# Kernel optimization log

Hardware: AMD Instinct MI355X
Metric: run time of the kernel (lower is better)

The kernel has to match this reference:

```python
import jax, jax.numpy as jnp
import numpy as np
from jax import lax

C = 256
HEADS = 8
AREA = 4
MLP_DIM = int(1.2 * C)  # 307


def _conv1x1(x, w, s, b):
    # x: [B,C,H,W], w: [O,C], s,b: [O]  (Conv2d 1x1 bias=False + folded BN)
    y = jnp.einsum('bchw,oc->bohw', x, w)
    return y * s[None, :, None, None] + b[None, :, None, None]


def _dwconv3x3(x, w, s, b):
    # depthwise 3x3, groups=C; w: [C,1,3,3]
    y = lax.conv_general_dilated(x, w, (1, 1), ((1, 1), (1, 1)),
                                 feature_group_count=x.shape[1],
                                 dimension_numbers=('NCHW', 'OIHW', 'NCHW'))
    return y * s[None, :, None, None] + b[None, :, None, None]


def setup_inputs() -> dict:
    key = jax.random.key(0)
    ks = jax.random.split(key, 8)
    B, H, W = 2, 64, 64
    x = jax.random.normal(ks[0], (B, C, H, W), dtype=jnp.float32)
    std = 0.02
    w_qk = jax.random.normal(ks[1], (2 * C, C), dtype=jnp.float32) * std
    w_v = jax.random.normal(ks[2], (C, C), dtype=jnp.float32) * std
    w_pe = jax.random.normal(ks[3], (C, 1, 3, 3), dtype=jnp.float32) * std
    w_proj = jax.random.normal(ks[4], (C, C), dtype=jnp.float32) * std
    w_m1 = jax.random.normal(ks[5], (MLP_DIM, C), dtype=jnp.float32) * std
    w_m2 = jax.random.normal(ks[6], (C, MLP_DIM), dtype=jnp.float32) * std
    ones = lambda n: jnp.ones((n,), jnp.float32)
    zeros = lambda n: jnp.zeros((n,), jnp.float32)
    return {
        'x': x,
        'w_qk': w_qk, 's_qk': ones(2 * C), 'b_qk': zeros(2 * C),
        'w_v': w_v, 's_v': ones(C), 'b_v': zeros(C),
        'w_pe': w_pe, 's_pe': ones(C), 'b_pe': zeros(C),
        'w_proj': w_proj, 's_proj': ones(C), 'b_proj': zeros(C),
        'w_m1': w_m1, 's_m1': ones(MLP_DIM), 'b_m1': zeros(MLP_DIM),
        'w_m2': w_m2, 's_m2': ones(C), 'b_m2': zeros(C),
    }


def _block(x, w_qk, s_qk, b_qk, w_v, s_v, b_v, w_pe, s_pe, b_pe,
           w_proj, s_proj, b_proj, w_m1, s_m1, b_m1, w_m2, s_m2, b_m2):
    B, Cc, H, W = x.shape
    N = H * W
    hd = Cc // HEADS
    scale = hd ** -0.5

    # --- AreaAttention ---
    qk = _conv1x1(x, w_qk, s_qk, b_qk).reshape(B, 2 * Cc, N)
    v4 = _conv1x1(x, w_v, s_v, b_v)                 # [B,C,H,W]
    pe = _dwconv3x3(v4, w_pe, s_pe, b_pe)           # positional encoding
    v = v4.reshape(B, Cc, N)

    # area split (row-major reshape, identical to torch contiguous reshape)
    Ba, Na = B * AREA, N // AREA
    qk = qk.reshape(Ba, 2 * Cc, Na)
    v = v.reshape(Ba, Cc, Na)
    q, k = qk[:, :Cc], qk[:, Cc:]
    q = q.reshape(Ba, HEADS, hd, Na)
    k = k.reshape(Ba, HEADS, hd, Na)
    v = v.reshape(Ba, HEADS, hd, Na)

    attn = jnp.einsum('bhdn,bhdm->bhnm', q, k) * scale  # [Ba,H,Na,Na]
    attn = jax.nn.softmax(attn, axis=-1)
    out = jnp.einsum('bhdm,bhnm->bhdn', v, attn)         # [Ba,H,hd,Na]

    out = out.reshape(B, Cc, N).reshape(B, Cc, H, W)
    attn_out = _conv1x1(out + pe, w_proj, s_proj, b_proj)

    x1 = x + attn_out  # add=True (shortcut and in_c==out_c)

    # --- conv2 MLP: Conv(SiLU) -> Conv(act=False) ---
    m = jax.nn.silu(_conv1x1(x1, w_m1, s_m1, b_m1))
    m = _conv1x1(m, w_m2, s_m2, b_m2)
    return x1 + m


def reference(x, w_qk, s_qk, b_qk, w_v, s_v, b_v, w_pe, s_pe, b_pe,
              w_proj, s_proj, b_proj, w_m1, s_m1, b_m1, w_m2, s_m2, b_m2):
    return _block(x, w_qk, s_qk, b_qk, w_v, s_v, b_v, w_pe, s_pe, b_pe,
                  w_proj, s_proj, b_proj, w_m1, s_m1, b_m1, w_m2, s_m2, b_m2)
```

## Files before the change

### kernel.cpp

```cpp
#include <hip/hip_runtime.h>

typedef __attribute__((ext_vector_type(8))) short s8v;
typedef __attribute__((ext_vector_type(4))) float f4v;

#define QSC (0.17677669529663687f * 1.4426950408889634f)

__device__ __forceinline__ unsigned short f2bf(float x) {
    unsigned u = __float_as_uint(x);
    return (unsigned short)((u + 0x7fffu + ((u >> 16) & 1u)) >> 16);
}
__device__ __forceinline__ float bf2f(unsigned short h) {
    return __uint_as_float(((unsigned)h) << 16);
}
__device__ __forceinline__ unsigned trunc2(float a, float b) {
    return (__float_as_uint(b) & 0xffff0000u) | (__float_as_uint(a) >> 16);
}

__global__ __launch_bounds__(256) void wconv_kernel(
    const float* __restrict__ wqk, const float* __restrict__ sqk, const float* __restrict__ bqk,
    const float* __restrict__ wv,  const float* __restrict__ sv,  const float* __restrict__ bv,
    const float* __restrict__ wprj, const float* __restrict__ sprj,
    const float* __restrict__ wm1, const float* __restrict__ sm1, const float* __restrict__ bm1,
    const float* __restrict__ wm2, const float* __restrict__ sm2,
    unsigned short* __restrict__ Wqkv, unsigned short* __restrict__ Wp,
    unsigned short* __restrict__ Wm1,  unsigned short* __restrict__ Wm2,
    float* __restrict__ bpad, float* __restrict__ bqv)
{
    int i = blockIdx.x * 256 + threadIdx.x;
    if (i < 196608) {
        int o = i >> 8, c = i & 255;
        float w;
        if (o < 512) { float f = ((o & 127) < 64) ? QSC : 1.f; w = wqk[i] * sqk[o] * f; }
        else          w = wv[(o - 512) * 256 + c] * sv[o - 512];
        Wqkv[i] = f2bf(w);
    } else if (i < 262144) {
        int j = i - 196608; int o = j >> 8; Wp[j] = f2bf(wprj[j] * sprj[o]);
    } else if (i < 360448) {
        int j = i - 262144; int o = j >> 8, c = j & 255;
        Wm1[j] = (o < 307) ? f2bf(wm1[o * 256 + c] * sm1[o]) : (unsigned short)0;
    } else if (i < 458752) {
        int j = i - 360448; int o = j / 384, c = j - o * 384;
        Wm2[j] = (c < 307) ? f2bf(wm2[o * 307 + c] * sm2[o]) : (unsigned short)0;
    } else if (i < 459136) {
        int j = i - 458752; bpad[j] = (j < 307) ? bm1[j] : 0.f;
    } else if (i < 459904) {
        int j = i - 459136;
        bqv[j] = (j < 512) ? (bqk[j] * (((j & 127) < 64) ? QSC : 1.f)) : bv[j - 512];
    }
}

__global__ __launch_bounds__(256) void mmqkv_kernel(
    const float* __restrict__ X, const unsigned short* __restrict__ Wb,
    const float* __restrict__ bi,
    unsigned short* __restrict__ qP, unsigned short* __restrict__ kP,
    unsigned short* __restrict__ vC, unsigned short* __restrict__ vT)
{
    __shared__ unsigned short Ap[64][40];
    __shared__ unsigned short Wt[128][40];
    const int tid = threadIdx.x, lane = tid & 63, wv = tid >> 6;
    const int lo4 = lane & 15, quad = lane >> 4;
    const int p0 = blockIdx.x * 64, o0 = blockIdx.y * 128, bB = blockIdx.z;
    const int ph = (wv & 1) * 32, oh = (wv >> 1) * 64;
    const int c2 = tid & 15, pg = tid >> 4;
    const int oW0 = tid >> 2, oW1 = (tid + 256) >> 2;
    const int cW = (tid & 3) * 8;
    const float* xb = X + (size_t)bB * 256 * 4096;

    f4v acc[4][2];
    #pragma unroll
    for (int i = 0; i < 4; i++)
        #pragma unroll
        for (int j = 0; j < 2; j++)
            acc[i][j] = (f4v){0.f, 0.f, 0.f, 0.f};

    float4 fa = *(const float4*)&xb[(size_t)(2 * c2) * 4096 + p0 + pg * 4];
    float4 fb = *(const float4*)&xb[(size_t)(2 * c2 + 1) * 4096 + p0 + pg * 4];
    uint4 wReg0 = *(const uint4*)(Wb + (size_t)(o0 + oW0) * 256 + cW);
    uint4 wReg1 = *(const uint4*)(Wb + (size_t)(o0 + oW1) * 256 + cW);

    for (int kc = 0; kc < 8; kc++) {
        __syncthreads();
        {
            float av[4] = {fa.x, fa.y, fa.z, fa.w};
            float bv2[4] = {fb.x, fb.y, fb.z, fb.w};
            #pragma unroll
            for (int i = 0; i < 4; i++)
                *(unsigned*)&Ap[pg * 4 + i][2 * c2] =
                    (unsigned)f2bf(av[i]) | ((unsigned)f2bf(bv2[i]) << 16);
        }
        *(uint4*)&Wt[oW0][cW] = wReg0;
        *(uint4*)&Wt[oW1][cW] = wReg1;
        __syncthreads();
        if (kc < 7) {
            int k1 = (kc + 1) * 32;
            fa = *(const float4*)&xb[(size_t)(k1 + 2 * c2) * 4096 + p0 + pg * 4];
            fb = *(const float4*)&xb[(size_t)(k1 + 2 * c2 + 1) * 4096 + p0 + pg * 4];
            wReg0 = *(const uint4*)(Wb + (size_t)(o0 + oW0) * 256 + k1 + cW);
            wReg1 = *(const uint4*)(Wb + (size_t)(o0 + oW1) * 256 + k1 + cW);
        }
        s8v af[4], bx[2];
        #pragma unroll
        for (int of = 0; of < 4; of++)
            af[of] = *(const s8v*)&Wt[oh + of * 16 + lo4][quad * 8];
        #pragma unroll
        for (int pf = 0; pf < 2; pf++)
            bx[pf] = *(const s8v*)&Ap[ph + pf * 16 + lo4][quad * 8];
        #pragma unroll
        for (int of = 0; of < 4; of++)
            #pragma unroll
            for (int pf = 0; pf < 2; pf++)
                acc[of][pf] = __builtin_amdgcn_mfma_f32_16x16x32_bf16(af[of], bx[pf], acc[of][pf], 0, 0, 0);
    }
    #pragma unroll
    for (int of = 0; of < 4; of++) {
        int ob = o0 + oh + of * 16 + quad * 4;
        float4 bb = *(const float4*)&bi[ob];
        float bbv[4] = {bb.x, bb.y, bb.z, bb.w};
        #pragma unroll
        for (int pf = 0; pf < 2; pf++) {
            int p = p0 + ph + pf * 16 + lo4;
            unsigned short b4[4];
            #pragma unroll
            for (int r = 0; r < 4; r++) b4[r] = f2bf(acc[of][pf][r] + bbv[r]);
            if (ob < 512) {
                int gg = ob >> 7, rr = ob & 127;
                int hh = (rr & 63) >> 3, j0 = rr & 7;
                unsigned short* dst = (rr >= 64) ? kP : qP;
                *(ushort4*)&dst[((((size_t)(bB * 4 + gg)) * 8 + hh) * 1024 + (p & 1023)) * 32
                                + (p >> 10) * 8 + j0] = *(ushort4*)b4;
            } else {
                *(ushort4*)&vC[((size_t)(bB * 4096 + p)) * 256 + (ob - 512)] = *(ushort4*)b4;
                #pragma unroll
                for (int r = 0; r < 4; r++)
                    vT[((size_t)(bB * 256 + ob - 512 + r)) * 4096 + p] = b4[r];
            }
        }
    }
}

__global__ __launch_bounds__(256) void attn_kernel(
    const unsigned short* __restrict__ qP, const unsigned short* __restrict__ kP,
    const unsigned short* __restrict__ vT,
    unsigned short* __restrict__ Opart, float* __restrict__ Lpart)
{
    __shared__ unsigned short Pq[4][32][72];
    const int tid = threadIdx.x;
    const int w = tid >> 6, lane = tid & 63;
    const int lo4 = lane & 15, quad = lane >> 4;
    const int n0 = blockIdx.z * 128;
    const int h = blockIdx.y;
    const int z = blockIdx.x;
    const int ba = z >> 2, spl = z & 3;
    const int bB = ba >> 2, g = ba & 3;
    const int mbase = spl * 256;

    const unsigned short* qb = qP + (((size_t)(bB * 4) + g) * 8 + h) * 32768;
    const unsigned short* kb = kP + (((size_t)(bB * 4) + g) * 8 + h) * 32768;

    s8v qf[2];
    #pragma unroll
    for (int qc = 0; qc < 2; qc++)
        qf[qc] = *(const s8v*)(qb + (size_t)(n0 + w * 32 + qc * 16 + lo4) * 32 + quad * 8);
    const int dd0 = lo4, dd1 = 16 + lo4;
    const unsigned short* vb0 = vT + ((size_t)(bB * 256 + g * 64 + h * 8 + (dd0 & 7))) * 4096 + (dd0 >> 3) * 1024 + mbase + quad * 8;
    const unsigned short* vb1 = vT + ((size_t)(bB * 256 + g * 64 + h * 8 + (dd1 & 7))) * 4096 + (dd1 >> 3) * 1024 + mbase + quad * 8;

    f4v oacc[2][2], Lacc[2];
    #pragma unroll
    for (int i = 0; i < 2; i++) {
        Lacc[i] = (f4v){0.f, 0.f, 0.f, 0.f};
        #pragma unroll
        for (int j = 0; j < 2; j++)
            oacc[i][j] = (f4v){0.f, 0.f, 0.f, 0.f};
    }
    s8v ones;
    #pragma unroll
    for (int j = 0; j < 8; j++) ones[j] = (short)0x3F80;

    s8v kf[4], vReg[2][2];
    #pragma unroll
    for (int mf = 0; mf < 4; mf++)
        kf[mf] = *(const s8v*)(kb + (size_t)(mbase + mf * 16 + lo4) * 32 + quad * 8);
    #pragma unroll
    for (int mc = 0; mc < 2; mc++) {
        vReg[mc][0] = *(const s8v*)(vb0 + mc * 32);
        vReg[mc][1] = *(const s8v*)(vb1 + mc * 32);
    }

    for (int sc = 0; sc < 4; sc++) {
        s8v kfn[4], vNext[2][2];
        if (sc < 3) {
            #pragma unroll
            for (int mf = 0; mf < 4; mf++)
                kfn[mf] = *(const s8v*)(kb + (size_t)(mbase + (sc + 1) * 64 + mf * 16 + lo4) * 32 + quad * 8);
            #pragma unroll
            for (int mc = 0; mc < 2; mc++) {
                vNext[mc][0] = *(const s8v*)(vb0 + (sc + 1) * 64 + mc * 32);
                vNext[mc][1] = *(const s8v*)(vb1 + (sc + 1) * 64 + mc * 32);
            }
        }
        f4v sT[4][2];
        #pragma unroll
        for (int mf = 0; mf < 4; mf++)
            #pragma unroll
            for (int qc = 0; qc < 2; qc++)
                sT[mf][qc] = __builtin_amdgcn_mfma_f32_16x16x32_bf16(kf[mf], qf[qc], (f4v){0.f, 0.f, 0.f, 0.f}, 0, 0, 0);
        #pragma unroll
        for (int qc = 0; qc < 2; qc++) {
            #pragma unroll
            for (int mf = 0; mf < 4; mf++) {
                float p0v = exp2f(sT[mf][qc][0]);
                float p1v = exp2f(sT[mf][qc][1]);
                float p2v = exp2f(sT[mf][qc][2]);
                float p3v = exp2f(sT[mf][qc][3]);
                uint2 pk;
                pk.x = trunc2(p0v, p1v);
                pk.y = trunc2(p2v, p3v);
                *(uint2*)&Pq[w][qc * 16 + lo4][mf * 16 + quad * 4] = pk;
            }
        }
        #pragma unroll
        for (int mc = 0; mc < 2; mc++) {
            s8v pfr[2];
            #pragma unroll
            for (int qc = 0; qc < 2; qc++)
                pfr[qc] = *(const s8v*)&Pq[w][qc * 16 + lo4][mc * 32 + quad * 8];
            #pragma unroll
            for (int df = 0; df < 2; df++)
                #pragma unroll
                for (int qc = 0; qc < 2; qc++)
                    oacc[df][qc] = __builtin_amdgcn_mfma_f32_16x16x32_bf16(vReg[mc][df], pfr[qc], oacc[df][qc], 0, 0, 0);
            #pragma unroll
            for (int qc = 0; qc < 2; qc++)
                Lacc[qc] = __builtin_amdgcn_mfma_f32_16x16x32_bf16(ones, pfr[qc], Lacc[qc], 0, 0, 0);
        }
        #pragma unroll
        for (int mf = 0; mf < 4; mf++) kf[mf] = kfn[mf];
        #pragma unroll
        for (int mc = 0; mc < 2; mc++) {
            vReg[mc][0] = vNext[mc][0];
            vReg[mc][1] = vNext[mc][1];
        }
    }
    if (quad == 0) {
        size_t lb = (((size_t)(spl * 2 + bB) * 4 + g) * 8 + h) * 1024 + n0 + w * 32;
        Lpart[lb + lo4] = Lacc[0][0];
        Lpart[lb + 16 + lo4] = Lacc[1][0];
    }
    #pragma unroll
    for (int qc = 0; qc < 2; qc++)
        #pragma unroll
        for (int df = 0; df < 2; df++) {
            int pb = df * 2 + (quad >> 1);
            uint2 ov;
            ov.x = trunc2(oacc[df][qc][0], oacc[df][qc][1]);
            ov.y = trunc2(oacc[df][qc][2], oacc[df][qc][3]);
            *(uint2*)(Opart + ((size_t)(spl * 2 + bB) * 4096 + pb * 1024 + n0 + w * 32 + qc * 16 + lo4) * 256
                      + g * 64 + h * 8 + (quad & 1) * 4) = ov;
        }
}

__global__ __launch_bounds__(256) void attpe_kernel(
    const unsigned short* __restrict__ Opart, const float* __restrict__ Lpart,
    const unsigned short* __restrict__ vC, const float* __restrict__ wpe,
    const float* __restrict__ spe, const float* __restrict__ bpe,
    unsigned short* __restrict__ attpe)
{
    int idx = blockIdx.x * 256 + threadIdx.x;
    int cg = (idx & 31) * 8;
    int p = (idx >> 5) & 4095;
    int bB = idx >> 17;
    float L = 0.f;
    float o[8] = {};
    #pragma unroll
    for (int spl = 0; spl < 4; spl++) {
        int g = cg >> 6, h = (cg >> 3) & 7;
        int na = p & 1023;
        L += Lpart[(((size_t)(spl * 2 + bB) * 4 + g) * 8 + h) * 1024 + na];
        uint4 v = *(const uint4*)(Opart + ((size_t)(spl * 2 + bB) * 4096 + p) * 256 + cg);
        unsigned short tmp[8]; *(uint4*)tmp = v;
        #pragma unroll
        for (int j = 0; j < 8; j++) o[j] += bf2f(tmp[j]);
    }
    float inv = 1.f / L;
    int hh = p >> 6, ww = p & 63;
    float pe[8] = {};
    for (int di = -1; di <= 1; di++) {
        int h2 = hh + di;
        if (h2 < 0 || h2 > 63) continue;
        for (int dj = -1; dj <= 1; dj++) {
            int w2 = ww + dj;
            if (w2 < 0 || w2 > 63) continue;
            uint4 vv = *(const uint4*)(vC + ((size_t)(bB * 4096 + h2 * 64 + w2)) * 256 + cg);
            unsigned short tmp[8]; *(uint4*)tmp = vv;
            int k = (di + 1) * 3 + (dj + 1);
            #pragma unroll
            for (int j = 0; j < 8; j++)
                pe[j] = fmaf(bf2f(tmp[j]), wpe[(cg + j) * 9 + k], pe[j]);
        }
    }
    unsigned short ob[8];
    #pragma unroll
    for (int j = 0; j < 8; j++)
        ob[j] = f2bf(o[j] * inv + pe[j] * spe[cg + j] + bpe[cg + j]);
    *(uint4*)(attpe + ((size_t)(bB * 4096 + p)) * 256 + cg) = *(uint4*)ob;
}

__global__ __launch_bounds__(256) void mlp3_kernel(
    const unsigned short* __restrict__ attpe, const float* __restrict__ x,
    const unsigned short* __restrict__ Wp, const float* __restrict__ bp,
    const unsigned short* __restrict__ Wm1, const float* __restrict__ bm1p,
    const unsigned short* __restrict__ Wm2, const float* __restrict__ bm2,
    float* __restrict__ out)
{
    __shared__ unsigned short bufA[32][392];
    __shared__ unsigned short bufX[32][264];
    const int tid = threadIdx.x, lane = tid & 63, wv = tid >> 6;
    const int lo4 = lane & 15, quad = lane >> 4;
    const int p0 = blockIdx.x * 32, bB = blockIdx.y;

    {
        int row = tid >> 3, cb = (tid & 7) * 32;
        const unsigned short* src = attpe + ((size_t)(bB * 4096 + p0 + row)) * 256 + cb;
        #pragma unroll
        for (int i = 0; i < 4; i++)
            *(uint4*)&bufA[row][cb + i * 8] = *(const uint4*)(src + i * 8);
    }
    __syncthreads();

    {
        f4v acc[4][2];
        #pragma unroll
        for (int i = 0; i < 4; i++)
            #pragma unroll
            for (int j = 0; j < 2; j++) acc[i][j] = (f4v){0.f, 0.f, 0.f, 0.f};
        for (int kk = 0; kk < 8; kk++) {
            s8v bx[2];
            #pragma unroll
            for (int pf = 0; pf < 2; pf++)
                bx[pf] = *(const s8v*)&bufA[pf * 16 + lo4][kk * 32 + quad * 8];
            #pragma unroll
            for (int of = 0; of < 4; of++) {
                s8v af = *(const s8v*)(Wp + (size_t)(wv * 64 + of * 16 + lo4) * 256 + kk * 32 + quad * 8);
                #pragma unroll
                for (int pf = 0; pf < 2; pf++)
                    acc[of][pf] = __builtin_amdgcn_mfma_f32_16x16x32_bf16(af, bx[pf], acc[of][pf], 0, 0, 0);
            }
        }
        #pragma unroll
        for (int of = 0; of < 4; of++) {
            int ob = wv * 64 + of * 16 + quad * 4;
            float4 bb = *(const float4*)&bp[ob];
            float bbv[4] = {bb.x, bb.y, bb.z, bb.w};
            #pragma unroll
            for (int pf = 0; pf < 2; pf++) {
                int p = p0 + pf * 16 + lo4;
                unsigned short b4[4];
                #pragma unroll
                for (int r = 0; r < 4; r++) {
                    float y = acc[of][pf][r] + bbv[r] + x[((size_t)(bB * 256 + ob + r)) * 4096 + p];
                    b4[r] = f2bf(y);
                }
                *(ushort4*)&bufX[pf * 16 + lo4][ob] = *(ushort4*)b4;
            }
        }
    }
    __syncthreads();

    {
        f4v acc[6][2];
        #pragma unroll
        for (int i = 0; i < 6; i++)
            #pragma unroll
            for (int j = 0; j < 2; j++) acc[i][j] = (f4v){0.f, 0.f, 0.f, 0.f};
        for (int kk = 0; kk < 8; kk++) {
            s8v bx[2];
            #pragma unroll
            for (int pf = 0; pf < 2; pf++)
                bx[pf] = *(const s8v*)&bufX[pf * 16 + lo4][kk * 32 + quad * 8];
            #pragma unroll
            for (int of = 0; of < 6; of++) {
                s8v af = *(const s8v*)(Wm1 + (size_t)(wv * 96 + of * 16 + lo4) * 256 + kk * 32 + quad * 8);
                #pragma unroll
                for (int pf = 0; pf < 2; pf++)
                    acc[of][pf] = __builtin_amdgcn_mfma_f32_16x16x32_bf16(af, bx[pf], acc[of][pf], 0, 0, 0);
            }
        }
        #pragma unroll
        for (int of = 0; of < 6; of++) {
            int ob = wv * 96 + of * 16 + quad * 4;
            float4 bb = *(const float4*)&bm1p[ob];
            float bbv[4] = {bb.x, bb.y, bb.z, bb.w};
            #pragma unroll
            for (int pf = 0; pf < 2; pf++) {
                unsigned short b4[4];
                #pragma unroll
                for (int r = 0; r < 4; r++) {
                    float y = acc[of][pf][r] + bbv[r];
                    y = y / (1.f + __expf(-y));
                    b4[r] = f2bf(y);
                }
                *(ushort4*)&bufA[pf * 16 + lo4][ob] = *(ushort4*)b4;
            }
        }
    }
    __syncthreads();

    {
        f4v acc[4][2];
        #pragma unroll
        for (int i = 0; i < 4; i++)
            #pragma unroll
            for (int j = 0; j < 2; j++) acc[i][j] = (f4v){0.f, 0.f, 0.f, 0.f};
        for (int kk = 0; kk < 12; kk++) {
            s8v bx[2];
            #pragma unroll
            for (int pf = 0; pf < 2; pf++)
                bx[pf] = *(const s8v*)&bufA[pf * 16 + lo4][kk * 32 + quad * 8];
            #pragma unroll
            for (int of = 0; of < 4; of++) {
                s8v af = *(const s8v*)(Wm2 + (size_t)(wv * 64 + of * 16 + lo4) * 384 + kk * 32 + quad * 8);
                #pragma unroll
                for (int pf = 0; pf < 2; pf++)
                    acc[of][pf] = __builtin_amdgcn_mfma_f32_16x16x32_bf16(af, bx[pf], acc[of][pf], 0, 0, 0);
            }
        }
        #pragma unroll
        for (int of = 0; of < 4; of++) {
            int ob = wv * 64 + of * 16 + quad * 4;
            float4 bb = *(const float4*)&bm2[ob];
            float bbv[4] = {bb.x, bb.y, bb.z, bb.w};
            #pragma unroll
            for (int pf = 0; pf < 2; pf++) {
                int p = p0 + pf * 16 + lo4;
                ushort4 x1v = *(const ushort4*)&bufX[pf * 16 + lo4][ob];
                unsigned short x1a[4]; *(ushort4*)x1a = x1v;
                #pragma unroll
                for (int r = 0; r < 4; r++) {
                    float y = acc[of][pf][r] + bbv[r] + bf2f(x1a[r]);
                    out[((size_t)(bB * 256 + ob + r)) * 4096 + p] = y;
                }
            }
        }
    }
}

extern "C" void kernel_launch(void* const* d_in, const int* in_sizes, int n_in,
                              void* d_out, int out_size, void* d_ws, size_t ws_size,
                              hipStream_t stream)
{
    const float* x      = (const float*)d_in[0];
    const float* w_qk   = (const float*)d_in[1];
    const float* s_qk   = (const float*)d_in[2];
    const float* b_qk   = (const float*)d_in[3];
    const float* w_v    = (const float*)d_in[4];
    const float* s_v    = (const float*)d_in[5];
    const float* b_v    = (const float*)d_in[6];
    const float* w_pe   = (const float*)d_in[7];
    const float* s_pe   = (const float*)d_in[8];
    const float* b_pe   = (const float*)d_in[9];
    const float* w_proj = (const float*)d_in[10];
    const float* s_proj = (const float*)d_in[11];
    const float* b_proj = (const float*)d_in[12];
    const float* w_m1   = (const float*)d_in[13];
    const float* s_m1   = (const float*)d_in[14];
    const float* b_m1   = (const float*)d_in[15];
    const float* w_m2   = (const float*)d_in[16];
    const float* s_m2   = (const float*)d_in[17];
    const float* b_m2   = (const float*)d_in[18];
    float* out = (float*)d_out;

    const size_t NA = (size_t)2 * 4096 * 256;
    unsigned short* attpe = (unsigned short*)d_ws;
    unsigned short* vC   = attpe + NA;
    unsigned short* qP   = vC + NA;
    unsigned short* kP   = qP + NA;
    unsigned short* Opart = kP + NA;
    float* Lpart = (float*)(Opart + 4 * NA);
    unsigned short* Wqkv = (unsigned short*)(Lpart + 262144);
    unsigned short* Wp   = Wqkv + 196608;
    unsigned short* Wm1  = Wp + 65536;
    unsigned short* Wm2  = Wm1 + 98304;
    float* bpad = (float*)(Wm2 + 98304);
    float* bqv  = bpad + 384;
    unsigned short* vT = (unsigned short*)(bqv + 768);

    dim3 blk(256);
    wconv_kernel<<<dim3(1797), blk, 0, stream>>>(
        w_qk, s_qk, b_qk, w_v, s_v, b_v, w_proj, s_proj,
        w_m1, s_m1, b_m1, w_m2, s_m2, Wqkv, Wp, Wm1, Wm2, bpad, bqv);

    mmqkv_kernel<<<dim3(64, 6, 2), blk, 0, stream>>>(x, Wqkv, bqv, qP, kP, vC, vT);

    attn_kernel<<<dim3(32, 8, 8), blk, 0, stream>>>(qP, kP, vT, Opart, Lpart);
    attpe_kernel<<<dim3(1024), blk, 0, stream>>>(Opart, Lpart, vC, w_pe, s_pe, b_pe, attpe);

    mlp3_kernel<<<dim3(128, 2), blk, 0, stream>>>(
        attpe, x, Wp, b_proj, Wm1, bpad, Wm2, b_m2, out);
}
```

Baseline: 201.2 us.

## Swizzle attention LDS, transpose PE weights, and retile MLP kernel to more blocks

Changes several kernels at once. The attention kernel drops the padded Pq layout in favour of an XOR-swizzled LDS layout, adds s_setprio around the MFMA bursts and fully unrolls the key loop. The depthwise PE weights are pre-transposed so attpe can use vector loads, and the per-channel scale and bias loads are vectorised. The MLP kernel now uses 16-pixel tiles with 512 threads over twice as many blocks, which raises parallelism but reloads the weights from global memory more often.

```diff
diff --git a/kernel.cpp b/kernel.cpp
--- a/kernel.cpp
+++ b/kernel.cpp
@@ -22,9 +22,10 @@
     const float* __restrict__ wprj, const float* __restrict__ sprj,
     const float* __restrict__ wm1, const float* __restrict__ sm1, const float* __restrict__ bm1,
     const float* __restrict__ wm2, const float* __restrict__ sm2,
+    const float* __restrict__ wpe9,
     unsigned short* __restrict__ Wqkv, unsigned short* __restrict__ Wp,
     unsigned short* __restrict__ Wm1,  unsigned short* __restrict__ Wm2,
-    float* __restrict__ bpad, float* __restrict__ bqv)
+    float* __restrict__ bpad, float* __restrict__ bqv, float* __restrict__ wpeT)
 {
     int i = blockIdx.x * 256 + threadIdx.x;
     if (i < 196608) {
@@ -46,6 +47,9 @@
     } else if (i < 459904) {
         int j = i - 459136;
         bqv[j] = (j < 512) ? (bqk[j] * (((j & 127) < 64) ? QSC : 1.f)) : bv[j - 512];
+    } else if (i < 462208) {
+        int j = i - 459904; int k = j >> 8, c = j & 255;
+        wpeT[j] = wpe9[c * 9 + k];
     }
 }
 
@@ -143,10 +147,11 @@
     const unsigned short* __restrict__ vT,
     unsigned short* __restrict__ Opart, float* __restrict__ Lpart)
 {
-    __shared__ unsigned short Pq[4][32][72];
+    __shared__ unsigned short Pq[4][32][64];
     const int tid = threadIdx.x;
     const int w = tid >> 6, lane = tid & 63;
     const int lo4 = lane & 15, quad = lane >> 4;
+    const int swz = (lo4 & 7) << 4;
     const int n0 = blockIdx.z * 128;
     const int h = blockIdx.y;
     const int z = blockIdx.x;
@@ -187,6 +192,7 @@
         vReg[mc][1] = *(const s8v*)(vb1 + mc * 32);
     }
 
+    #pragma unroll
     for (int sc = 0; sc < 4; sc++) {
         s8v kfn[4], vNext[2][2];
         if (sc < 3) {
@@ -200,13 +206,16 @@
             }
         }
         f4v sT[4][2];
+        __builtin_amdgcn_s_setprio(1);
         #pragma unroll
         for (int mf = 0; mf < 4; mf++)
             #pragma unroll
             for (int qc = 0; qc < 2; qc++)
                 sT[mf][qc] = __builtin_amdgcn_mfma_f32_16x16x32_bf16(kf[mf], qf[qc], (f4v){0.f, 0.f, 0.f, 0.f}, 0, 0, 0);
+        __builtin_amdgcn_s_setprio(0);
         #pragma unroll
         for (int qc = 0; qc < 2; qc++) {
+            char* prow = (char*)&Pq[w][qc * 16 + lo4][0];
             #pragma unroll
             for (int mf = 0; mf < 4; mf++) {
                 float p0v = exp2f(sT[mf][qc][0]);
@@ -216,7 +225,7 @@
                 uint2 pk;
                 pk.x = trunc2(p0v, p1v);
                 pk.y = trunc2(p2v, p3v);
-                *(uint2*)&Pq[w][qc * 16 + lo4][mf * 16 + quad * 4] = pk;
+                *(uint2*)(prow + ((mf * 32 + quad * 8) ^ swz)) = pk;
             }
         }
         #pragma unroll
@@ -224,7 +233,8 @@
             s8v pfr[2];
             #pragma unroll
             for (int qc = 0; qc < 2; qc++)
-                pfr[qc] = *(const s8v*)&Pq[w][qc * 16 + lo4][mc * 32 + quad * 8];
+                pfr[qc] = *(const s8v*)((const char*)&Pq[w][qc * 16 + lo4][0] + ((mc * 64 + quad * 16) ^ swz));
+            __builtin_amdgcn_s_setprio(1);
             #pragma unroll
             for (int df = 0; df < 2; df++)
                 #pragma unroll
@@ -233,13 +243,16 @@
             #pragma unroll
             for (int qc = 0; qc < 2; qc++)
                 Lacc[qc] = __builtin_amdgcn_mfma_f32_16x16x32_bf16(ones, pfr[qc], Lacc[qc], 0, 0, 0);
-        }
-        #pragma unroll
-        for (int mf = 0; mf < 4; mf++) kf[mf] = kfn[mf];
-        #pragma unroll
-        for (int mc = 0; mc < 2; mc++) {
-            vReg[mc][0] = vNext[mc][0];
-            vReg[mc][1] = vNext[mc][1];
+            __builtin_amdgcn_s_setprio(0);
+        }
+        if (sc < 3) {
+            #pragma unroll
+            for (int mf = 0; mf < 4; mf++) kf[mf] = kfn[mf];
+            #pragma unroll
+            for (int mc = 0; mc < 2; mc++) {
+                vReg[mc][0] = vNext[mc][0];
+                vReg[mc][1] = vNext[mc][1];
+            }
         }
     }
     if (quad == 0) {
@@ -262,7 +275,7 @@
 
 __global__ __launch_bounds__(256) void attpe_kernel(
     const unsigned short* __restrict__ Opart, const float* __restrict__ Lpart,
-    const unsigned short* __restrict__ vC, const float* __restrict__ wpe,
+    const unsigned short* __restrict__ vC, const float* __restrict__ wpeT,
     const float* __restrict__ spe, const float* __restrict__ bpe,
     unsigned short* __restrict__ attpe)
 {
@@ -270,12 +283,12 @@
     int cg = (idx & 31) * 8;
     int p = (idx >> 5) & 4095;
     int bB = idx >> 17;
+    int g = cg >> 6, h = (cg >> 3) & 7;
+    int na = p & 1023;
     float L = 0.f;
     float o[8] = {};
     #pragma unroll
     for (int spl = 0; spl < 4; spl++) {
-        int g = cg >> 6, h = (cg >> 3) & 7;
-        int na = p & 1023;
         L += Lpart[(((size_t)(spl * 2 + bB) * 4 + g) * 8 + h) * 1024 + na];
         uint4 v = *(const uint4*)(Opart + ((size_t)(spl * 2 + bB) * 4096 + p) * 256 + cg);
         unsigned short tmp[8]; *(uint4*)tmp = v;
@@ -294,152 +307,122 @@
             uint4 vv = *(const uint4*)(vC + ((size_t)(bB * 4096 + h2 * 64 + w2)) * 256 + cg);
             unsigned short tmp[8]; *(uint4*)tmp = vv;
             int k = (di + 1) * 3 + (dj + 1);
+            float4 wa = *(const float4*)&wpeT[k * 256 + cg];
+            float4 wb = *(const float4*)&wpeT[k * 256 + cg + 4];
+            float ww8[8] = {wa.x, wa.y, wa.z, wa.w, wb.x, wb.y, wb.z, wb.w};
             #pragma unroll
             for (int j = 0; j < 8; j++)
-                pe[j] = fmaf(bf2f(tmp[j]), wpe[(cg + j) * 9 + k], pe[j]);
-        }
-    }
+                pe[j] = fmaf(bf2f(tmp[j]), ww8[j], pe[j]);
+        }
+    }
+    float4 sa = *(const float4*)&spe[cg];
+    float4 sb = *(const float4*)&spe[cg + 4];
+    float4 b0 = *(const float4*)&bpe[cg];
+    float4 b1 = *(const float4*)&bpe[cg + 4];
+    float sv8[8] = {sa.x, sa.y, sa.z, sa.w, sb.x, sb.y, sb.z, sb.w};
+    float bv8[8] = {b0.x, b0.y, b0.z, b0.w, b1.x, b1.y, b1.z, b1.w};
     unsigned short ob[8];
     #pragma unroll
     for (int j = 0; j < 8; j++)
-        ob[j] = f2bf(o[j] * inv + pe[j] * spe[cg + j] + bpe[cg + j]);
+        ob[j] = f2bf(o[j] * inv + pe[j] * sv8[j] + bv8[j]);
     *(uint4*)(attpe + ((size_t)(bB * 4096 + p)) * 256 + cg) = *(uint4*)ob;
 }
 
-__global__ __launch_bounds__(256) void mlp3_kernel(
+__global__ __launch_bounds__(512) void mlp3_kernel(
     const unsigned short* __restrict__ attpe, const float* __restrict__ x,
     const unsigned short* __restrict__ Wp, const float* __restrict__ bp,
     const unsigned short* __restrict__ Wm1, const float* __restrict__ bm1p,
     const unsigned short* __restrict__ Wm2, const float* __restrict__ bm2,
     float* __restrict__ out)
 {
-    __shared__ unsigned short bufA[32][392];
-    __shared__ unsigned short bufX[32][264];
+    __shared__ unsigned short bufA[16][392];
+    __shared__ unsigned short bufX[16][264];
     const int tid = threadIdx.x, lane = tid & 63, wv = tid >> 6;
     const int lo4 = lane & 15, quad = lane >> 4;
-    const int p0 = blockIdx.x * 32, bB = blockIdx.y;
+    const int p0 = blockIdx.x * 16, bB = blockIdx.y;
 
     {
-        int row = tid >> 3, cb = (tid & 7) * 32;
-        const unsigned short* src = attpe + ((size_t)(bB * 4096 + p0 + row)) * 256 + cb;
-        #pragma unroll
-        for (int i = 0; i < 4; i++)
-            *(uint4*)&bufA[row][cb + i * 8] = *(const uint4*)(src + i * 8);
+        int row = tid >> 5, cb = (tid & 31) * 8;
+        *(uint4*)&bufA[row][cb] =
+            *(const uint4*)(attpe + ((size_t)(bB * 4096 + p0 + row)) * 256 + cb);
     }
     __syncthreads();
 
     {
-        f4v acc[4][2];
-        #pragma unroll
-        for (int i = 0; i < 4; i++)
-            #pragma unroll
-            for (int j = 0; j < 2; j++) acc[i][j] = (f4v){0.f, 0.f, 0.f, 0.f};
+        f4v acc[2] = {(f4v){0.f, 0.f, 0.f, 0.f}, (f4v){0.f, 0.f, 0.f, 0.f}};
         for (int kk = 0; kk < 8; kk++) {
-            s8v bx[2];
-            #pragma unroll
-            for (int pf = 0; pf < 2; pf++)
-                bx[pf] = *(const s8v*)&bufA[pf * 16 + lo4][kk * 32 + quad * 8];
-            #pragma unroll
-            for (int of = 0; of < 4; of++) {
-                s8v af = *(const s8v*)(Wp + (size_t)(wv * 64 + of * 16 + lo4) * 256 + kk * 32 + quad * 8);
-                #pragma unroll
-                for (int pf = 0; pf < 2; pf++)
-                    acc[of][pf] = __builtin_amdgcn_mfma_f32_16x16x32_bf16(af, bx[pf], acc[of][pf], 0, 0, 0);
-            }
-        }
-        #pragma unroll
-        for (int of = 0; of < 4; of++) {
-            int ob = wv * 64 + of * 16 + quad * 4;
+            s8v bx = *(const s8v*)&bufA[lo4][kk * 32 + quad * 8];
+            #pragma unroll
+            for (int of = 0; of < 2; of++) {
+                s8v af = *(const s8v*)(Wp + (size_t)(wv * 32 + of * 16 + lo4) * 256 + kk * 32 + quad * 8);
+                acc[of] = __builtin_amdgcn_mfma_f32_16x16x32_bf16(af, bx, acc[of], 0, 0, 0);
+            }
+        }
+        #pragma unroll
+        for (int of = 0; of < 2; of++) {
+            int ob = wv * 32 + of * 16 + quad * 4;
             float4 bb = *(const float4*)&bp[ob];
             float bbv[4] = {bb.x, bb.y, bb.z, bb.w};
-            #pragma unroll
-            for (int pf = 0; pf < 2; pf++) {
-                int p = p0 + pf * 16 + lo4;
-                unsigned short b4[4];
-                #pragma unroll
-                for (int r = 0; r < 4; r++) {
-                    float y = acc[of][pf][r] + bbv[r] + x[((size_t)(bB * 256 + ob + r)) * 4096 + p];
-                    b4[r] = f2bf(y);
-                }
-                *(ushort4*)&bufX[pf * 16 + lo4][ob] = *(ushort4*)b4;
-            }
+            int p = p0 + lo4;
+            unsigned short b4[4];
+            #pragma unroll
+            for (int r = 0; r < 4; r++) {
+                float y = acc[of][r] + bbv[r] + x[((size_t)(bB * 256 + ob + r)) * 4096 + p];
+                b4[r] = f2bf(y);
+            }
+            *(ushort4*)&bufX[lo4][ob] = *(ushort4*)b4;
         }
     }
     __syncthreads();
 
     {
-        f4v acc[6][2];
-        #pragma unroll
-        for (int i = 0; i < 6; i++)
-            #pragma unroll
-            for (int j = 0; j < 2; j++) acc[i][j] = (f4v){0.f, 0.f, 0.f, 0.f};
+        f4v acc[3] = {(f4v){0.f, 0.f, 0.f, 0.f}, (f4v){0.f, 0.f, 0.f, 0.f}, (f4v){0.f, 0.f, 0.f, 0.f}};
         for (int kk = 0; kk < 8; kk++) {
-            s8v bx[2];
-            #pragma unroll
-            for (int pf = 0; pf < 2; pf++)
-                bx[pf] = *(const s8v*)&bufX[pf * 16 + lo4][kk * 32 + quad * 8];
-            #pragma unroll
-            for (int of = 0; of < 6; of++) {
-                s8v af = *(const s8v*)(Wm1 + (size_t)(wv * 96 + of * 16 + lo4) * 256 + kk * 32 + quad * 8);
-                #pragma unroll
-                for (int pf = 0; pf < 2; pf++)
-                    acc[of][pf] = __builtin_amdgcn_mfma_f32_16x16x32_bf16(af, bx[pf], acc[of][pf], 0, 0, 0);
-            }
-        }
-        #pragma unroll
-        for (int of = 0; of < 6; of++) {
-            int ob = wv * 96 + of * 16 + quad * 4;
+            s8v bx = *(const s8v*)&bufX[lo4][kk * 32 + quad * 8];
+            #pragma unroll
+            for (int of = 0; of < 3; of++) {
+                s8v af = *(const s8v*)(Wm1 + (size_t)(wv * 48 + of * 16 + lo4) * 256 + kk * 32 + quad * 8);
+                acc[of] = __builtin_amdgcn_mfma_f32_16x16x32_bf16(af, bx, acc[of], 0, 0, 0);
+            }
+        }
+        #pragma unroll
+        for (int of = 0; of < 3; of++) {
+            int ob = wv * 48 + of * 16 + quad * 4;
             float4 bb = *(const float4*)&bm1p[ob];
             float bbv[4] = {bb.x, bb.y, bb.z, bb.w};
-            #pragma unroll
-            for (int pf = 0; pf < 2; pf++) {
-                unsigned short b4[4];
-                #pragma unroll
-                for (int r = 0; r < 4; r++) {
-                    float y = acc[of][pf][r] + bbv[r];
-                    y = y / (1.f + __expf(-y));
-                    b4[r] = f2bf(y);
-                }
-                *(ushort4*)&bufA[pf * 16 + lo4][ob] = *(ushort4*)b4;
-            }
+            unsigned short b4[4];
+            #pragma unroll
+            for (int r = 0; r < 4; r++) {
+                float y = acc[of][r] + bbv[r];
+                y = y / (1.f + __expf(-y));
+                b4[r] = f2bf(y);
+            }
+            *(ushort4*)&bufA[lo4][ob] = *(ushort4*)b4;
         }
     }
     __syncthreads();
 
     {
-        f4v acc[4][2];
-        #pragma unroll
-        for (int i = 0; i < 4; i++)
-            #pragma unroll
-            for (int j = 0; j < 2; j++) acc[i][j] = (f4v){0.f, 0.f, 0.f, 0.f};
+        f4v acc[2] = {(f4v){0.f, 0.f, 0.f, 0.f}, (f4v){0.f, 0.f, 0.f, 0.f}};
         for (int kk = 0; kk < 12; kk++) {
-            s8v bx[2];
-            #pragma unroll
-            for (int pf = 0; pf < 2; pf++)
-                bx[pf] = *(const s8v*)&bufA[pf * 16 + lo4][kk * 32 + quad * 8];
-            #pragma unroll
-            for (int of = 0; of < 4; of++) {
-                s8v af = *(const s8v*)(Wm2 + (size_t)(wv * 64 + of * 16 + lo4) * 384 + kk * 32 + quad * 8);
-                #pragma unroll
-                for (int pf = 0; pf < 2; pf++)
-                    acc[of][pf] = __builtin_amdgcn_mfma_f32_16x16x32_bf16(af, bx[pf], acc[of][pf], 0, 0, 0);
-            }
-        }
-        #pragma unroll
-        for (int of = 0; of < 4; of++) {
-            int ob = wv * 64 + of * 16 + quad * 4;
+            s8v bx = *(const s8v*)&bufA[lo4][kk * 32 + quad * 8];
+            #pragma unroll
+            for (int of = 0; of < 2; of++) {
+                s8v af = *(const s8v*)(Wm2 + (size_t)(wv * 32 + of * 16 + lo4) * 384 + kk * 32 + quad * 8);
+                acc[of] = __builtin_amdgcn_mfma_f32_16x16x32_bf16(af, bx, acc[of], 0, 0, 0);
+            }
+        }
+        #pragma unroll
+        for (int of = 0; of < 2; of++) {
+            int ob = wv * 32 + of * 16 + quad * 4;
             float4 bb = *(const float4*)&bm2[ob];
             float bbv[4] = {bb.x, bb.y, bb.z, bb.w};
-            #pragma unroll
-            for (int pf = 0; pf < 2; pf++) {
-                int p = p0 + pf * 16 + lo4;
-                ushort4 x1v = *(const ushort4*)&bufX[pf * 16 + lo4][ob];
-                unsigned short x1a[4]; *(ushort4*)x1a = x1v;
-                #pragma unroll
-                for (int r = 0; r < 4; r++) {
-                    float y = acc[of][pf][r] + bbv[r] + bf2f(x1a[r]);
-                    out[((size_t)(bB * 256 + ob + r)) * 4096 + p] = y;
-                }
+            ushort4 x1v = *(const ushort4*)&bufX[lo4][ob];
+            unsigned short x1a[4]; *(ushort4*)x1a = x1v;
+            #pragma unroll
+            for (int r = 0; r < 4; r++) {
+                float y = acc[of][r] + bbv[r] + bf2f(x1a[r]);
+                out[((size_t)(bB * 256 + ob + r)) * 4096 + p0 + lo4] = y;
             }
         }
     }
@@ -483,18 +466,20 @@
     unsigned short* Wm2  = Wm1 + 98304;
     float* bpad = (float*)(Wm2 + 98304);
     float* bqv  = bpad + 384;
-    unsigned short* vT = (unsigned short*)(bqv + 768);
+    float* wpeT = bqv + 768;
+    unsigned short* vT = (unsigned short*)(wpeT + 2304);
 
     dim3 blk(256);
-    wconv_kernel<<<dim3(1797), blk, 0, stream>>>(
+    wconv_kernel<<<dim3(1806), blk, 0, stream>>>(
         w_qk, s_qk, b_qk, w_v, s_v, b_v, w_proj, s_proj,
-        w_m1, s_m1, b_m1, w_m2, s_m2, Wqkv, Wp, Wm1, Wm2, bpad, bqv);
+        w_m1, s_m1, b_m1, w_m2, s_m2, w_pe,
+        Wqkv, Wp, Wm1, Wm2, bpad, bqv, wpeT);
 
     mmqkv_kernel<<<dim3(64, 6, 2), blk, 0, stream>>>(x, Wqkv, bqv, qP, kP, vC, vT);
 
     attn_kernel<<<dim3(32, 8, 8), blk, 0, stream>>>(qP, kP, vT, Opart, Lpart);
-    attpe_kernel<<<dim3(1024), blk, 0, stream>>>(Opart, Lpart, vC, w_pe, s_pe, b_pe, attpe);
-
-    mlp3_kernel<<<dim3(128, 2), blk, 0, stream>>>(
+    attpe_kernel<<<dim3(1024), blk, 0, stream>>>(Opart, Lpart, vC, wpeT, s_pe, b_pe, attpe);
+
+    mlp3_kernel<<<dim3(256, 2), dim3(512), 0, stream>>>(
         attpe, x, Wp, b_proj, Wm1, bpad, Wm2, b_m2, out);
 }
```

New measurement: 180.0 us. 1.12x faster.
